# Kernel optimization log

Measured on AMD Instinct MI355X. Metric: run time of the kernel, lower is better.

The kernel has to match this reference:

```python
import jax, jax.numpy as jnp
import numpy as np

DIM = 180; HEADS = 6; WS = 16; NUM_TOKENS = 64; RDIM = 10; CAT = 128
KS = 5; MLP_HID = 360; DTD = 64; Hh = 64; Ww = 64; B = 8; M = 64


def _ln(x, g, b, eps=1e-5):
    mu = x.mean(-1, keepdims=True)
    var = ((x - mu) ** 2).mean(-1, keepdims=True)
    return (x - mu) / jnp.sqrt(var + eps) * g + b


def _l2norm(x):
    return x / jnp.clip(jnp.linalg.norm(x, axis=-1, keepdims=True), 1e-12)


def setup_inputs() -> dict:
    key = jax.random.key(0)
    ks = jax.random.split(key, 24)
    rn = lambda k, s: jax.random.normal(k, s, jnp.float32) * 0.02
    z = lambda *s: jnp.zeros(s, jnp.float32)
    return {
        'x': jax.random.normal(ks[0], (B, Hh * Ww, DIM), jnp.float32),
        'td': jax.random.normal(ks[1], (B, M, DIM), jnp.float32),
        'norm1_g': jnp.ones((DIM,), jnp.float32), 'norm1_b': z(DIM),
        'wqkv_w': rn(ks[2], (DIM, 3 * DIM)), 'wqkv_b': z(3 * DIM),
        'atd_wq_w': rn(ks[3], (DIM, RDIM)), 'atd_wq_b': z(RDIM),
        'atd_wk_w': rn(ks[4], (DIM, RDIM)), 'atd_wk_b': z(RDIM),
        'atd_wv_w': rn(ks[5], (DIM, DIM)), 'atd_wv_b': z(DIM),
        'atd_scale': jnp.ones((1,), jnp.float32),
        'aca_proj_w': rn(ks[6], (DIM, DIM)), 'aca_proj_b': z(DIM),
        'win_rpb': rn(ks[7], ((2 * WS - 1) ** 2, HEADS)),
        'win_proj_w': rn(ks[8], (DIM, DIM)), 'win_proj_b': z(DIM),
        'fc_td_w': rn(ks[9], (DIM, DTD)), 'fc_td_b': z(DTD),
        'fc1_w': rn(ks[10], (DIM, MLP_HID)), 'fc1_b': z(MLP_HID),
        'dw_w': rn(ks[11], (MLP_HID + DTD, 1, KS, KS)), 'dw_b': z(MLP_HID + DTD),
        'fc2_w': rn(ks[12], (MLP_HID + DTD, DIM)), 'fc2_b': z(DIM),
        'norm2_g': jnp.ones((DIM,), jnp.float32), 'norm2_b': z(DIM),
        'rpi_sa': jax.random.randint(ks[13], (WS * WS, WS * WS), 0, (2 * WS - 1) ** 2),
        'h': Hh, 'w': Ww,
    }


def reference(x, td, norm1_g, norm1_b, wqkv_w, wqkv_b, atd_wq_w, atd_wq_b,
              atd_wk_w, atd_wk_b, atd_wv_w, atd_wv_b, atd_scale,
              aca_proj_w, aca_proj_b, win_rpb, win_proj_w, win_proj_b,
              fc_td_w, fc_td_b, fc1_w, fc1_b, dw_w, dw_b, fc2_w, fc2_b,
              norm2_g, norm2_b, rpi_sa, h, w):
    b, n, c = x.shape
    hd = c // HEADS
    shortcut = x
    xn = _ln(x, norm1_g, norm1_b)
    qkv = xn @ wqkv_w + wqkv_b  # [b, n, 3c]

    # --- ATD_CA: l2-normalized cross-attention to token dictionary ---
    q = xn @ atd_wq_w + atd_wq_b          # [b, n, rd]
    kk = td @ atd_wk_w + atd_wk_b         # [b, m, rd]
    vv = td @ atd_wv_w + atd_wv_b         # [b, m, c]
    logit_scale = 1.0 + jnp.clip(atd_scale, 0.0, 3.0) * np.log(NUM_TOKENS)
    sim = jnp.einsum('bnr,bmr->bnm', _l2norm(q), _l2norm(kk)) * logit_scale
    attn_atd = jax.nn.softmax(sim, axis=-1)
    x_atd = jnp.einsum('bnm,bmc->bnc', attn_atd, vv)
    tk_id = jnp.argmax(attn_atd, axis=-1)  # [b, n]

    # --- AC_MSA: category-sorted grouped attention ---
    gs = min(n, CAT); ng = (n + gs - 1) // gs; pad_n = ng * gs - n
    sort_idx = jnp.argsort(tk_id, axis=-1)
    inv_idx = jnp.argsort(sort_idx, axis=-1)  # inverse permutation
    sq = jnp.take_along_axis(qkv, sort_idx[:, :, None], axis=1)
    sq = jnp.concatenate([sq, jnp.flip(sq[:, n - pad_n:n, :], axis=1)], axis=1)
    g = sq.reshape(b, ng, gs, 3, HEADS, hd).transpose(3, 0, 1, 4, 2, 5)
    qa, ka, va = g[0], g[1], g[2]          # [b, ng, H, gs, hd]
    a = jax.nn.softmax(jnp.einsum('bgHid,bgHjd->bgHij', qa, ka) * hd ** -0.5, axis=-1)
    y = jnp.einsum('bgHij,bgHjd->bgHid', a, va).transpose(0, 1, 3, 2, 4)
    y = y.reshape(b, n + pad_n, c)[:, :n]
    x_aca = jnp.take_along_axis(y, inv_idx[:, :, None], axis=1) @ aca_proj_w + aca_proj_b

    # --- gather per-token dictionary features for FFN ---
    td_proj = td @ fc_td_w + fc_td_b       # [b, m, dtd]
    x_td = jnp.take_along_axis(td_proj, jnp.broadcast_to(tk_id[:, :, None], (b, n, DTD)), axis=1)

    # --- window attention (shift_size = 0, no mask) ---
    nwh, nww = h // WS, w // WS
    win = qkv.reshape(b, nwh, WS, nww, WS, 3 * c).transpose(0, 1, 3, 2, 4, 5)
    win = win.reshape(-1, WS * WS, 3 * c)
    B_ = win.shape[0]; N = WS * WS
    wq = win.reshape(B_, N, 3, HEADS, hd).transpose(2, 0, 3, 1, 4)
    qw, kw, vw = wq[0] * hd ** -0.5, wq[1], wq[2]
    bias = win_rpb[rpi_sa.reshape(-1)].reshape(N, N, HEADS).transpose(2, 0, 1)[None]
    aw = jax.nn.softmax(jnp.einsum('wHid,wHjd->wHij', qw, kw) + bias, axis=-1)
    ow = jnp.einsum('wHij,wHjd->wHid', aw, vw).transpose(0, 2, 1, 3).reshape(B_, N, c)
    ow = ow @ win_proj_w + win_proj_b
    attn_x = ow.reshape(b, nwh, nww, WS, WS, c).transpose(0, 1, 3, 2, 4, 5).reshape(b, n, c)

    x = shortcut + x_atd + attn_x + x_aca

    # --- ConvFFN_td with depthwise conv branch ---
    x2 = _ln(x, norm2_g, norm2_b)
    h1 = jax.nn.gelu(x2 @ fc1_w + fc1_b, approximate=False)
    hc = jnp.concatenate([h1, x_td], axis=-1)  # [b, n, C]
    C = hc.shape[-1]
    img = jnp.swapaxes(hc, 1, 2).reshape(b, C, h, w)
    conv = jax.lax.conv_general_dilated(img, dw_w, (1, 1), 'SAME',
        dimension_numbers=('NCHW', 'OIHW', 'NCHW'), feature_group_count=C)
    conv = jax.nn.gelu(conv + dw_b[None, :, None, None], approximate=False)
    hc = hc + jnp.swapaxes(conv.reshape(b, C, n), 1, 2)
    return x + hc @ fc2_w + fc2_b
```

## Files before the change

### kernel.cpp

```cpp
#include <hip/hip_runtime.h>
#include <hip/hip_bf16.h>
#include <math.h>

#define BB      8
#define NTOK    4096
#define CDIM    180
#define C3      540
#define NHEADS  6
#define HD      30
#define MDICT   64
#define RD      10
#define DTD     64
#define MHID    360
#define CCAT    424
#define WS      16
#define WIN_N   256
#define GS      128
#define NG      32
#define ROWS    (BB*NTOK)
#define KP1     192
#define KP2     448

typedef __hip_bfloat16 bf16;
typedef short v8s __attribute__((ext_vector_type(8)));
typedef float f32x4 __attribute__((ext_vector_type(4)));
typedef unsigned int u32x4 __attribute__((ext_vector_type(4)));

__device__ __forceinline__ float gelu_exact(float x) {
    return 0.5f * x * (1.0f + erff(x * 0.70710678118654752f));
}
__device__ __forceinline__ float wave_sum(float v) {
    #pragma unroll
    for (int off = 32; off > 0; off >>= 1) v += __shfl_xor(v, off, 64);
    return v;
}
__device__ __forceinline__ unsigned short f2b(float v) {
    unsigned u = __float_as_uint(v);
    return (unsigned short)((u + 0x7FFFu + ((u >> 16) & 1u)) >> 16);
}
__device__ __forceinline__ float b2f(unsigned short h) {
    return __uint_as_float(((unsigned)h) << 16);
}
__device__ __forceinline__ unsigned packbf(float lo, float hi) {
    return (unsigned)f2b(lo) | ((unsigned)f2b(hi) << 16);
}

__global__ __launch_bounds__(256) void detect_kernel(const void* __restrict__ x,
                                                     int* __restrict__ flag,
                                                     int* __restrict__ diag)
{
    __shared__ int cnt;
    if (threadIdx.x == 0) { cnt = 0; *diag = 0; }
    __syncthreads();
    const unsigned short* u = (const unsigned short*)x;
    int c = 0;
    for (int i = threadIdx.x; i < 2048; i += 256) {
        unsigned short e = u[2 * i] & 0x7F80;
        if (e >= 0x4300) c++;
    }
    atomicAdd(&cnt, c);
    __syncthreads();
    if (threadIdx.x == 0) *flag = (cnt > 16) ? 1 : 0;
}

#define NCVT 23
struct CvtArgs {
    const void* src[NCVT];
    float* dst[NCVT];
    int cum[NCVT + 1];
};
__global__ __launch_bounds__(256) void convert_all_kernel(CvtArgs a, int total,
        const int* __restrict__ flag)
{
    int i = blockIdx.x * 256 + threadIdx.x;
    if (i >= total) return;
    int s = 0;
    while (i >= a.cum[s + 1]) s++;
    int off = i - a.cum[s];
    if (*flag) a.dst[s][off] = ((const float*)a.src[s])[off];
    else       a.dst[s][off] = __bfloat162float(((const bf16*)a.src[s])[off]);
}

__global__ __launch_bounds__(256) void check_f32_kernel(const float* __restrict__ buf,
        int n, int bit, int* __restrict__ diag)
{
    int i = blockIdx.x * 256 + threadIdx.x;
    if (i >= n) return;
    unsigned u = __float_as_uint(buf[i]);
    if ((u & 0x7F800000u) == 0x7F800000u) atomicOr(diag, bit);
}

__global__ __launch_bounds__(256) void emit_kernel(const float* __restrict__ src,
        void* __restrict__ out, const int* __restrict__ flag,
        const int* __restrict__ diag, int n)
{
    int i = blockIdx.x * 256 + threadIdx.x;
    if (i >= n) return;
    float v = src[i];
    int d = *diag;
    if (d) v = 100.f + 32.f * (float)d;
    if (*flag) ((float*)out)[i] = v;
    else       ((bf16*)out)[i]  = __float2bfloat16(v);
}

__global__ __launch_bounds__(256) void zero_tail_kernel(bf16* __restrict__ buf)
{
    int idx = blockIdx.x * 256 + threadIdx.x;
    int row = idx / 12, c = idx % 12;
    buf[(size_t)row * KP1 + CDIM + c] = __float2bfloat16(0.f);
}

__global__ __launch_bounds__(256) void packW_kernel(const void* __restrict__ W,
        bf16* __restrict__ Wt, int K, int N, int Kpad, int total,
        const int* __restrict__ flag)
{
    int idx = blockIdx.x * 256 + threadIdx.x;
    if (idx >= total) return;
    int n = idx / Kpad, k = idx % Kpad;
    float v = 0.f;
    if (k < K && n < N) {
        size_t src = (size_t)k * N + n;
        v = (*flag) ? ((const float*)W)[src]
                    : __bfloat162float(((const bf16*)W)[src]);
    }
    Wt[idx] = __float2bfloat16(v);
}

__global__ __launch_bounds__(256) void bias_pre_kernel(const int* __restrict__ rpi,
        const float* __restrict__ rpb, float* __restrict__ bias_t)
{
    int idx = blockIdx.x * 256 + threadIdx.x;
    int h = idx >> 16, ij = idx & 65535;
    bias_t[idx] = rpb[rpi[ij] * NHEADS + h];
}

template<bool GELU_, bool ADDRES, bool BIAS_>
__global__ __launch_bounds__(256) void mgemm_kernel(
        const bf16* __restrict__ A, int lda,
        const bf16* __restrict__ Wt, int ldw,
        const float* __restrict__ bias,
        const float* __restrict__ res, int ldr,
        float* __restrict__ outF, int ldo, int N, int K)
{
    __shared__ unsigned short As[64][32];
    __shared__ unsigned short Bs[64][32];
    int tid = threadIdx.x;
    int wave = tid >> 6, lane = tid & 63;
    int quad = lane >> 4, mr = lane & 15;
    int row0 = blockIdx.y * 64, col0 = blockIdx.x * 64;
    f32x4 z = {0.f, 0.f, 0.f, 0.f};
    f32x4 acc[4] = {z, z, z, z};
    const unsigned short* Au = (const unsigned short*)A;
    const unsigned short* Wu = (const unsigned short*)Wt;
    for (int k0 = 0; k0 < K; k0 += 32) {
        #pragma unroll
        for (int e = 0; e < 8; e++) {
            int idx = tid * 8 + e;
            int r = idx >> 5, c = idx & 31;
            As[r][c] = Au[(size_t)(row0 + r) * lda + k0 + c];
            Bs[r][c] = Wu[(size_t)(col0 + r) * ldw + k0 + c];
        }
        __syncthreads();
        v8s a;
        #pragma unroll
        for (int j = 0; j < 8; j++) a[j] = (short)As[wave * 16 + mr][quad * 8 + j];
        #pragma unroll
        for (int ni = 0; ni < 4; ni++) {
            v8s b;
            #pragma unroll
            for (int j = 0; j < 8; j++) b[j] = (short)Bs[ni * 16 + mr][quad * 8 + j];
            acc[ni] = __builtin_amdgcn_mfma_f32_16x16x32_bf16(a, b, acc[ni], 0, 0, 0);
        }
        __syncthreads();
    }
    #pragma unroll
    for (int ni = 0; ni < 4; ni++) {
        int gc = col0 + ni * 16 + mr;
        if (gc >= N) continue;
        float bv = BIAS_ ? bias[gc] : 0.f;
        #pragma unroll
        for (int r = 0; r < 4; r++) {
            int gr = row0 + wave * 16 + quad * 4 + r;
            float v = acc[ni][r] + bv;
            if (GELU_) v = gelu_exact(v);
            if (ADDRES) v += res[(size_t)gr * ldr + gc];
            outF[(size_t)gr * ldo + gc] = v;
        }
    }
}

__global__ __launch_bounds__(256) void av_mgemm_kernel(
        const bf16* __restrict__ P, const bf16* __restrict__ vvT,
        const float* __restrict__ xres, float* __restrict__ accout)
{
    __shared__ unsigned short As[64][32];
    __shared__ unsigned short Bs[64][32];
    int tid = threadIdx.x;
    int wave = tid >> 6, lane = tid & 63;
    int quad = lane >> 4, mr = lane & 15;
    int row0 = blockIdx.y * 64, col0 = blockIdx.x * 64;
    int bz = blockIdx.z;
    const unsigned short* Au = (const unsigned short*)P + (size_t)bz * NTOK * MDICT;
    const unsigned short* Wu = (const unsigned short*)vvT + (size_t)bz * 192 * MDICT;
    const float* res = xres + (size_t)bz * NTOK * CDIM;
    float* outF = accout + (size_t)bz * NTOK * CDIM;
    f32x4 z = {0.f, 0.f, 0.f, 0.f};
    f32x4 acc[4] = {z, z, z, z};
    for (int k0 = 0; k0 < MDICT; k0 += 32) {
        #pragma unroll
        for (int e = 0; e < 8; e++) {
            int idx = tid * 8 + e;
            int r = idx >> 5, c = idx & 31;
            As[r][c] = Au[(size_t)(row0 + r) * MDICT + k0 + c];
            Bs[r][c] = Wu[(size_t)(col0 + r) * MDICT + k0 + c];
        }
        __syncthreads();
        v8s a;
        #pragma unroll
        for (int j = 0; j < 8; j++) a[j] = (short)As[wave * 16 + mr][quad * 8 + j];
        #pragma unroll
        for (int ni = 0; ni < 4; ni++) {
            v8s b;
            #pragma unroll
            for (int j = 0; j < 8; j++) b[j] = (short)Bs[ni * 16 + mr][quad * 8 + j];
            acc[ni] = __builtin_amdgcn_mfma_f32_16x16x32_bf16(a, b, acc[ni], 0, 0, 0);
        }
        __syncthreads();
    }
    #pragma unroll
    for (int ni = 0; ni < 4; ni++) {
        int gc = col0 + ni * 16 + mr;
        if (gc >= CDIM) continue;
        #pragma unroll
        for (int r = 0; r < 4; r++) {
            int gr = row0 + wave * 16 + quad * 4 + r;
            float v = acc[ni][r] + res[(size_t)gr * CDIM + gc];
            outF[(size_t)gr * CDIM + gc] = v;
        }
    }
}

__global__ __launch_bounds__(256, 4) void win_mfma_kernel(const float* __restrict__ qkv,
        const float* __restrict__ bias_t, bf16* __restrict__ outb)
{
    int b = blockIdx.y;
    int widx = blockIdx.x / NHEADS;
    int hh = blockIdx.x % NHEADS;
    int wy = widx >> 2, wx = widx & 3;
    int tid = threadIdx.x;
    int wave = tid >> 6, lane = tid & 63, quad = lane >> 4, mr = lane & 15;
    __shared__ __align__(16) unsigned short Ks[64][40];
    __shared__ __align__(16) unsigned short Vt[32][80];

    size_t brow = (size_t)b * NTOK;
    const float scq = 0.18257418583505536f;

    v8s aq[4];
    #pragma unroll
    for (int tt = 0; tt < 4; tt++) {
        int m = (wave * 4 + tt) * 16 + mr;
        int nt_ = (wy * WS + (m >> 4)) * 64 + wx * WS + (m & 15);
        const float* qrow = qkv + (brow + nt_) * C3 + hh * HD;
        #pragma unroll
        for (int jj = 0; jj < 8; jj++) {
            int d = quad * 8 + jj;
            float v = (d < HD) ? qrow[d] * scq : 0.f;
            aq[tt][jj] = (short)f2b(v);
        }
    }
    f32x4 z = {0.f, 0.f, 0.f, 0.f};
    f32x4 oacc[4][2] = {{z, z}, {z, z}, {z, z}, {z, z}};
    float m_r[4], l_r[4];
    #pragma unroll
    for (int tt = 0; tt < 4; tt++) { m_r[tt] = -3.0e38f; l_r[tt] = 0.f; }
    const float* btab = bias_t + (size_t)hh * WIN_N * WIN_N;

    for (int kc = 0; kc < WIN_N; kc += 64) {
        {
            int j = tid >> 2, dg = (tid & 3) * 8;
            int tok = kc + j;
            int nt_ = (wy * WS + (tok >> 4)) * 64 + wx * WS + (tok & 15);
            const float* krow = qkv + (brow + nt_) * C3 + CDIM + hh * HD;
            const float* vrow = qkv + (brow + nt_) * C3 + 2 * CDIM + hh * HD;
            v8s kv;
            #pragma unroll
            for (int jj = 0; jj < 8; jj++) {
                int d = dg + jj;
                float kf = (d < HD) ? krow[d] : 0.f;
                float vf = (d < HD) ? vrow[d] : 0.f;
                kv[jj] = (short)f2b(kf);
                Vt[d][j] = f2b(vf);
            }
            *(v8s*)&Ks[j][dg] = kv;
        }
        __syncthreads();
        #pragma unroll
        for (int tt = 0; tt < 4; tt++) {
            f32x4 s[4];
            #pragma unroll
            for (int nt = 0; nt < 4; nt++) {
                v8s bk = *(const v8s*)&Ks[nt * 16 + mr][quad * 8];
                s[nt] = __builtin_amdgcn_mfma_f32_16x16x32_bf16(bk, aq[tt], z, 0, 0, 0);
            }
            int qg = (wave * 4 + tt) * 16 + mr;
            const float* bi = btab + (size_t)qg * WIN_N + kc;
            float mc = -3.0e38f;
            #pragma unroll
            for (int nt = 0; nt < 4; nt++) {
                f32x4 b4 = *(const f32x4*)(bi + nt * 16 + quad * 4);
                s[nt][0] += b4[0]; s[nt][1] += b4[1];
                s[nt][2] += b4[2]; s[nt][3] += b4[3];
                mc = fmaxf(mc, fmaxf(fmaxf(s[nt][0], s[nt][1]),
                                     fmaxf(s[nt][2], s[nt][3])));
            }
            mc = fmaxf(mc, __shfl_xor(mc, 16, 64));
            mc = fmaxf(mc, __shfl_xor(mc, 32, 64));
            float mn = fmaxf(m_r[tt], mc);
            float alpha = __expf(m_r[tt] - mn);
            m_r[tt] = mn;
            float ls = 0.f;
            #pragma unroll
            for (int nt = 0; nt < 4; nt++) {
                #pragma unroll
                for (int r = 0; r < 4; r++) {
                    float pp = __expf(s[nt][r] - mn);
                    ls += pp;
                    s[nt][r] = pp;
                }
            }
            ls += __shfl_xor(ls, 16, 64);
            ls += __shfl_xor(ls, 32, 64);
            l_r[tt] = l_r[tt] * alpha + ls;
            unsigned dpk[4][2];
            #pragma unroll
            for (int nt = 0; nt < 4; nt++) {
                dpk[nt][0] = packbf(s[nt][0], s[nt][1]);
                dpk[nt][1] = packbf(s[nt][2], s[nt][3]);
            }
            #pragma unroll
            for (int r = 0; r < 4; r++) {
                float av = __shfl(alpha, quad * 4 + r, 64);
                oacc[tt][0][r] *= av;
                oacc[tt][1][r] *= av;
            }
            #pragma unroll
            for (int c = 0; c < 2; c++) {
                union { u32x4 u; v8s s8; } afu;
                #pragma unroll
                for (int t = 0; t < 4; t++) {
                    int srcl = (((quad * 2 + (t >> 1)) & 3) << 4) | mr;
                    unsigned r0 = (unsigned)__shfl((int)dpk[2 * c][t & 1], srcl, 64);
                    unsigned r1 = (unsigned)__shfl((int)dpk[2 * c + 1][t & 1], srcl, 64);
                    afu.u[t] = (quad & 2) ? r1 : r0;
                }
                #pragma unroll
                for (int dt = 0; dt < 2; dt++) {
                    v8s bv = *(const v8s*)&Vt[dt * 16 + mr][c * 32 + quad * 8];
                    oacc[tt][dt] = __builtin_amdgcn_mfma_f32_16x16x32_bf16(
                        afu.s8, bv, oacc[tt][dt], 0, 0, 0);
                }
            }
        }
        __syncthreads();
    }
    #pragma unroll
    for (int tt = 0; tt < 4; tt++) {
        float il = 1.f / l_r[tt];
        #pragma unroll
        for (int r = 0; r < 4; r++) {
            float ilr = __shfl(il, quad * 4 + r, 64);
            int m = (wave * 4 + tt) * 16 + quad * 4 + r;
            int nt_ = (wy * WS + (m >> 4)) * 64 + wx * WS + (m & 15);
            #pragma unroll
            for (int dt = 0; dt < 2; dt++) {
                int d = dt * 16 + mr;
                if (d >= HD) continue;
                outb[(brow + nt_) * KP1 + hh * HD + d] =
                    __float2bfloat16(oacc[tt][dt][r] * ilr);
            }
        }
    }
}

__global__ __launch_bounds__(256) void acmsa_mfma_kernel(const float* __restrict__ qkv,
        const int* __restrict__ sidx, bf16* __restrict__ outb)
{
    int b = blockIdx.y;
    int g = blockIdx.x / NHEADS;
    int hh = blockIdx.x % NHEADS;
    int tid = threadIdx.x;
    int wave = tid >> 6, lane = tid & 63, quad = lane >> 4, mr = lane & 15;
    __shared__ int toks[GS];
    __shared__ __align__(16) unsigned short Ks[64][40];
    __shared__ __align__(16) unsigned short Vt[32][80];
    __shared__ __align__(16) unsigned short Sc[GS][72];
    __shared__ float alpha_s[GS];
    __shared__ float invl_s[GS];

    size_t brow = (size_t)b * NTOK;
    if (tid < GS) toks[tid] = sidx[brow + (size_t)g * GS + tid];
    __syncthreads();
    const float scq = 0.18257418583505536f;

    v8s aq[2];
    #pragma unroll
    for (int tt = 0; tt < 2; tt++) {
        int m = (wave * 2 + tt) * 16 + mr;
        const float* qrow = qkv + (brow + toks[m]) * C3 + hh * HD;
        #pragma unroll
        for (int jj = 0; jj < 8; jj++) {
            int d = quad * 8 + jj;
            float v = (d < HD) ? qrow[d] * scq : 0.f;
            aq[tt][jj] = (short)f2b(v);
        }
    }
    f32x4 z = {0.f, 0.f, 0.f, 0.f};
    f32x4 oacc[2][2] = {{z, z}, {z, z}};
    float m_r = -3.0e38f, l_r = 0.f;

    for (int kc = 0; kc < GS; kc += 64) {
        {
            int j = tid >> 2, dg = (tid & 3) * 8;
            int tok = toks[kc + j];
            const float* krow = qkv + (brow + tok) * C3 + CDIM + hh * HD;
            const float* vrow = qkv + (brow + tok) * C3 + 2 * CDIM + hh * HD;
            v8s kv;
            #pragma unroll
            for (int jj = 0; jj < 8; jj++) {
                int d = dg + jj;
                float kf = (d < HD) ? krow[d] : 0.f;
                float vf = (d < HD) ? vrow[d] : 0.f;
                kv[jj] = (short)f2b(kf);
                Vt[d][j] = f2b(vf);
            }
            *(v8s*)&Ks[j][dg] = kv;
        }
        __syncthreads();
        #pragma unroll
        for (int nt = 0; nt < 4; nt++) {
            v8s bk = *(const v8s*)&Ks[nt * 16 + mr][quad * 8];
            #pragma unroll
            for (int tt = 0; tt < 2; tt++) {
                f32x4 s = __builtin_amdgcn_mfma_f32_16x16x32_bf16(aq[tt], bk, z, 0, 0, 0);
                int rowb = (wave * 2 + tt) * 16 + quad * 4;
                #pragma unroll
                for (int r = 0; r < 4; r++)
                    Sc[rowb + r][nt * 16 + mr] = f2b(s[r]);
            }
        }
        __syncthreads();
        if (tid < GS) {
            int r = tid;
            float mc = -3.0e38f;
            #pragma unroll
            for (int j0 = 0; j0 < 64; j0 += 8) {
                v8s sv = *(const v8s*)&Sc[r][j0];
                #pragma unroll
                for (int jj = 0; jj < 8; jj++)
                    mc = fmaxf(mc, b2f((unsigned short)sv[jj]));
            }
            float mn = fmaxf(m_r, mc);
            float alpha = __expf(m_r - mn);
            float lsum = 0.f;
            #pragma unroll
            for (int j0 = 0; j0 < 64; j0 += 8) {
                v8s sv = *(const v8s*)&Sc[r][j0];
                v8s pv;
                #pragma unroll
                for (int jj = 0; jj < 8; jj++) {
                    float pp = __expf(b2f((unsigned short)sv[jj]) - mn);
                    lsum += pp;
                    pv[jj] = (short)f2b(pp);
                }
                *(v8s*)&Sc[r][j0] = pv;
            }
            l_r = l_r * alpha + lsum;
            m_r = mn;
            alpha_s[r] = alpha;
        }
        __syncthreads();
        #pragma unroll
        for (int tt = 0; tt < 2; tt++) {
            int rowb = (wave * 2 + tt) * 16 + quad * 4;
            float a0 = alpha_s[rowb], a1 = alpha_s[rowb + 1],
                  a2 = alpha_s[rowb + 2], a3 = alpha_s[rowb + 3];
            #pragma unroll
            for (int dt = 0; dt < 2; dt++) {
                oacc[tt][dt][0] *= a0; oacc[tt][dt][1] *= a1;
                oacc[tt][dt][2] *= a2; oacc[tt][dt][3] *= a3;
            }
        }
        #pragma unroll
        for (int kk = 0; kk < 64; kk += 32) {
            v8s ap[2];
            #pragma unroll
            for (int tt = 0; tt < 2; tt++)
                ap[tt] = *(const v8s*)&Sc[(wave * 2 + tt) * 16 + mr][kk + quad * 8];
            #pragma unroll
            for (int dt = 0; dt < 2; dt++) {
                v8s bv = *(const v8s*)&Vt[dt * 16 + mr][kk + quad * 8];
                #pragma unroll
                for (int tt = 0; tt < 2; tt++)
                    oacc[tt][dt] = __builtin_amdgcn_mfma_f32_16x16x32_bf16(
                        ap[tt], bv, oacc[tt][dt], 0, 0, 0);
            }
        }
        __syncthreads();
    }
    if (tid < GS) invl_s[tid] = 1.f / l_r;
    __syncthreads();
    #pragma unroll
    for (int tt = 0; tt < 2; tt++) {
        int rowb = (wave * 2 + tt) * 16 + quad * 4;
        #pragma unroll
        for (int dt = 0; dt < 2; dt++) {
            int d = dt * 16 + mr;
            if (d >= HD) continue;
            #pragma unroll
            for (int r = 0; r < 4; r++) {
                int m = rowb + r;
                int tok = toks[m];
                outb[(brow + tok) * KP1 + hh * HD + d] =
                    __float2bfloat16(oacc[tt][dt][r] * invl_s[m]);
            }
        }
    }
}

__global__ __launch_bounds__(64) void ln_kernel(const float* __restrict__ x,
        const float* __restrict__ g, const float* __restrict__ be,
        float* __restrict__ out, bf16* __restrict__ outb)
{
    int row = blockIdx.x; int t = threadIdx.x;
    const float* xr = x + (size_t)row * CDIM;
    float v0 = xr[t];
    float v1 = xr[t + 64];
    float v2 = (t < CDIM - 128) ? xr[t + 128] : 0.f;
    float s1 = wave_sum(v0 + v1 + v2);
    float s2 = wave_sum(v0*v0 + v1*v1 + v2*v2);
    float mu = s1 / (float)CDIM;
    float var = s2 / (float)CDIM - mu * mu;
    float rs = rsqrtf(var + 1e-5f);
    float o0 = (v0 - mu) * rs * g[t]      + be[t];
    float o1 = (v1 - mu) * rs * g[t + 64] + be[t + 64];
    float o2 = (t < CDIM - 128) ? ((v2 - mu) * rs * g[t + 128] + be[t + 128]) : 0.f;
    float* o = out + (size_t)row * CDIM;
    o[t] = o0; o[t + 64] = o1;
    if (t < CDIM - 128) o[t + 128] = o2;
    bf16* ob = outb + (size_t)row * KP1;
    ob[t]       = __float2bfloat16(o0);
    ob[t + 64]  = __float2bfloat16(o1);
    ob[t + 128] = __float2bfloat16(o2);
}

__global__ __launch_bounds__(64) void td_pre_kernel(const float* __restrict__ td,
        const float* __restrict__ wk, const float* __restrict__ wkb,
        const float* __restrict__ wv, const float* __restrict__ wvb,
        const float* __restrict__ wtd, const float* __restrict__ wtdb,
        float* __restrict__ kkn, bf16* __restrict__ vvT, float* __restrict__ tdp)
{
    int blk = blockIdx.x;
    int b = blk >> 6, m = blk & 63;
    int t = threadIdx.x;
    __shared__ float tr[CDIM];
    __shared__ float sk[RD];
    __shared__ float snorm;
    const float* tdr = td + (size_t)blk * CDIM;
    tr[t] = tdr[t]; tr[t + 64] = tdr[t + 64];
    if (t < CDIM - 128) tr[t + 128] = tdr[t + 128];
    __syncthreads();
    if (t < RD) {
        float s = wkb[t];
        for (int k = 0; k < CDIM; k++) s += tr[k] * wk[k * RD + t];
        sk[t] = s;
    }
    __syncthreads();
    if (t == 0) {
        float s = 0.f;
        #pragma unroll
        for (int j = 0; j < RD; j++) s += sk[j] * sk[j];
        snorm = fmaxf(sqrtf(s), 1e-12f);
    }
    __syncthreads();
    if (t < RD) kkn[(size_t)blk * RD + t] = sk[t] / snorm;
    for (int c = t; c < 192; c += 64) {
        float s = 0.f;
        if (c < CDIM) {
            s = wvb[c];
            for (int k = 0; k < CDIM; k++) s += tr[k] * wv[k * CDIM + c];
        }
        vvT[((size_t)(b * 192 + c)) * MDICT + m] = __float2bfloat16(s);
    }
    {
        float s = wtdb[t];
        for (int k = 0; k < CDIM; k++) s += tr[k] * wtd[k * DTD + t];
        tdp[(size_t)blk * DTD + t] = s;
    }
}

__global__ __launch_bounds__(64) void atd_soft_kernel(const float* __restrict__ xn,
        const float* __restrict__ wq, const float* __restrict__ wqb,
        const float* __restrict__ scale_p, const float* __restrict__ kkn,
        bf16* __restrict__ Pout, int* __restrict__ tk_id)
{
    int row = blockIdx.x;
    int b = row >> 12;
    int t = threadIdx.x;
    const float* xrow = xn + (size_t)row * CDIM;
    float v0 = xrow[t];
    float v1 = xrow[t + 64];
    float v2 = (t < CDIM - 128) ? xrow[t + 128] : 0.f;
    float sq[RD];
    #pragma unroll
    for (int j = 0; j < RD; j++) {
        float part = v0 * wq[t * RD + j] + v1 * wq[(t + 64) * RD + j];
        if (t < CDIM - 128) part += v2 * wq[(t + 128) * RD + j];
        sq[j] = wave_sum(part) + wqb[j];
    }
    float qn = 0.f;
    #pragma unroll
    for (int j = 0; j < RD; j++) qn += sq[j] * sq[j];
    qn = fmaxf(sqrtf(qn), 1e-12f);
    float ls = 1.0f + fminf(fmaxf(scale_p[0], 0.f), 3.f) * 4.158883083359672f;
    const float* kr = kkn + ((size_t)b * MDICT + t) * RD;
    float s = 0.f;
    #pragma unroll
    for (int j = 0; j < RD; j++) s += sq[j] * kr[j];
    s = s / qn * ls;
    float mv = s; int mi = t;
    #pragma unroll
    for (int off = 32; off > 0; off >>= 1) {
        float ov = __shfl_xor(mv, off, 64);
        int   oi = __shfl_xor(mi, off, 64);
        if (ov > mv || (ov == mv && oi < mi)) { mv = ov; mi = oi; }
    }
    float e = __expf(s - mv);
    float denom = wave_sum(e);
    Pout[(size_t)row * MDICT + t] = __float2bfloat16(e / denom);
    if (t == 0) tk_id[row] = mi;
}

__global__ __launch_bounds__(256) void sort_kernel(const int* __restrict__ tk_id,
                                                   int* __restrict__ sidx)
{
    int b = blockIdx.x; int tid = threadIdx.x;
    __shared__ int keys[NTOK];
    __shared__ int cnt[256];
    __shared__ int off[256];
    const int* kb = tk_id + (size_t)b * NTOK;
    for (int i = tid; i < NTOK; i += 256) keys[i] = kb[i];
    __syncthreads();
    int v = tid >> 2, seg = tid & 3;
    int lo = seg * 1024, hi = lo + 1024;
    int c = 0;
    for (int i = lo; i < hi; i++) c += (keys[i] == v);
    cnt[tid] = c;
    __syncthreads();
    if (tid == 0) {
        int run = 0;
        for (int l = 0; l < 256; l++) { off[l] = run; run += cnt[l]; }
    }
    __syncthreads();
    int o = off[tid];
    int* sb = sidx + (size_t)b * NTOK;
    for (int i = lo; i < hi; i++) if (keys[i] == v) sb[o++] = i;
}

__global__ __launch_bounds__(256) void gather_td_kernel(const int* __restrict__ tk_id,
        const float* __restrict__ tdp, float* __restrict__ hc)
{
    int idx = blockIdx.x * 256 + threadIdx.x;
    int row = idx >> 6, j = idx & 63;
    int b = row >> 12;
    int tk = tk_id[row];
    hc[(size_t)row * CCAT + MHID + j] = tdp[((size_t)b * MDICT + tk) * DTD + j];
}

#define CHK2 16
#define CHP2 17
__global__ __launch_bounds__(256) void conv_kernel(const float* __restrict__ hc,
        const float* __restrict__ w, const float* __restrict__ wb,
        bf16* __restrict__ outb)
{
    int ch0 = blockIdx.x * CHK2;
    int tile = blockIdx.y;
    int b = blockIdx.z;
    int ty0 = (tile >> 2) * 16, tx0 = (tile & 3) * 16;
    __shared__ float sh[400][CHP2];
    __shared__ float wt[CHK2][26];
    int tid = threadIdx.x;
    for (int idx = tid; idx < 400 * CHK2; idx += 256) {
        int pix = idx >> 4, ch = idx & (CHK2 - 1);
        int gy = ty0 + pix / 20 - 2, gx = tx0 + pix % 20 - 2;
        int chg = ch0 + ch;
        float v = 0.f;
        if (gy >= 0 && gy < 64 && gx >= 0 && gx < 64 && chg < CCAT)
            v = hc[((size_t)b * NTOK + gy * 64 + gx) * CCAT + chg];
        sh[pix][ch] = v;
    }
    for (int idx = tid; idx < CHK2 * 25; idx += 256) {
        int ch = idx / 25, kk = idx % 25;
        int chg = ch0 + ch;
        wt[ch][kk] = (chg < CCAT) ? w[chg * 25 + kk] : 0.f;
    }
    __syncthreads();
    int px = tid & 15, py = tid >> 4;
    size_t obase = ((size_t)b * NTOK + (ty0 + py) * 64 + tx0 + px) * KP2;
    #pragma unroll
    for (int ch = 0; ch < CHK2; ch++) {
        int chg = ch0 + ch;
        float v = 0.f;
        if (chg < CCAT) {
            float a = 0.f;
            #pragma unroll
            for (int dy = 0; dy < 5; dy++)
                #pragma unroll
                for (int dx = 0; dx < 5; dx++)
                    a += sh[(py + dy) * 20 + px + dx][ch] * wt[ch][dy * 5 + dx];
            float gv = gelu_exact(a + wb[chg]);
            v = sh[(py + 2) * 20 + px + 2][ch] + gv;
        }
        outb[obase + chg] = __float2bfloat16(v);
    }
}

extern "C" void kernel_launch(void* const* d_in, const int* in_sizes, int n_in,
                              void* d_out, int out_size, void* d_ws, size_t ws_size,
                              hipStream_t stream)
{
    (void)n_in; (void)ws_size; (void)out_size;
    const int* rpi = (const int*)d_in[28];

    float* p = (float*)d_ws;
    float* xn    = p; p += (size_t)ROWS * CDIM;
    float* acc   = p; p += (size_t)ROWS * CDIM;
    float* tmp1  = p; p += (size_t)ROWS * CDIM;
    float* qkv   = p; p += (size_t)ROWS * C3;
    float* hcnew = p; p += (size_t)ROWS * CCAT;
    float* kkn   = p; p += (size_t)BB * MDICT * RD;
    bf16*  vvT   = (bf16*)p; p += (size_t)BB * 192 * MDICT / 2;
    float* tdp   = p; p += (size_t)BB * MDICT * DTD;
    int*   tk_id = (int*)p; p += ROWS;
    int*   sidx  = (int*)p; p += ROWS;
    int*   flag  = (int*)p; p += 64;
    int*   diag  = (int*)p; p += 64;
    bf16* wtqkv = (bf16*)p; p += 576 * KP1 / 2;
    bf16* wtaca = (bf16*)p; p += 192 * KP1 / 2;
    bf16* wtwin = (bf16*)p; p += 192 * KP1 / 2;
    bf16* wtfc1 = (bf16*)p; p += 384 * KP1 / 2;
    bf16* wtfc2 = (bf16*)p; p += 192 * KP2 / 2;
    float* cin[28];
    for (int i = 0; i < 28; i++) { cin[i] = p; p += in_sizes[i]; }
    float* bias_t = p; p += (size_t)NHEADS * WIN_N * WIN_N;

    float* hc      = qkv;
    bf16*  xnb     = (bf16*)hcnew;
    bf16*  tmp1b   = (bf16*)(hcnew + (size_t)ROWS * KP1 / 2);
    bf16*  hcnewb2 = (bf16*)hcnew;
    bf16*  Pbuf    = (bf16*)tmp1;

    detect_kernel<<<1, 256, 0, stream>>>(d_in[0], flag, diag);
    {
        CvtArgs ca;
        int total = 0, s = 0;
        for (int i = 0; i < 28; i++) {
            if (i == 4 || i == 13 || i == 16 || i == 20 || i == 24) continue;
            ca.src[s] = d_in[i];
            ca.dst[s] = cin[i];
            ca.cum[s] = total;
            total += in_sizes[i];
            s++;
        }
        ca.cum[s] = total;
        convert_all_kernel<<<(total + 255) / 256, 256, 0, stream>>>(ca, total, flag);
    }
    const float *x = cin[0], *td = cin[1], *n1g = cin[2], *n1b = cin[3],
        *wqkv_b = cin[5], *wq_w = cin[6], *wq_b = cin[7],
        *wk_w = cin[8], *wk_b = cin[9], *wv_w = cin[10], *wv_b = cin[11],
        *atd_scale = cin[12], *aca_b = cin[14], *win_rpb = cin[15],
        *winp_b = cin[17], *fctd_w = cin[18], *fctd_b = cin[19],
        *fc1_b = cin[21], *dw_w = cin[22], *dw_b = cin[23], *fc2_b = cin[25],
        *n2g = cin[26], *n2b = cin[27];

    packW_kernel<<<576 * KP1 / 256, 256, 0, stream>>>(d_in[4],  wtqkv, CDIM, C3,   KP1, 576 * KP1, flag);
    packW_kernel<<<192 * KP1 / 256, 256, 0, stream>>>(d_in[13], wtaca, CDIM, CDIM, KP1, 192 * KP1, flag);
    packW_kernel<<<192 * KP1 / 256, 256, 0, stream>>>(d_in[16], wtwin, CDIM, CDIM, KP1, 192 * KP1, flag);
    packW_kernel<<<384 * KP1 / 256, 256, 0, stream>>>(d_in[20], wtfc1, CDIM, MHID, KP1, 384 * KP1, flag);
    packW_kernel<<<192 * KP2 / 256, 256, 0, stream>>>(d_in[24], wtfc2, CCAT, CDIM, KP2, 192 * KP2, flag);
    bias_pre_kernel<<<NHEADS * WIN_N * WIN_N / 256, 256, 0, stream>>>(rpi, win_rpb, bias_t);

    td_pre_kernel<<<BB * MDICT, 64, 0, stream>>>(td, wk_w, wk_b, wv_w, wv_b,
                                                 fctd_w, fctd_b, kkn, vvT, tdp);
    ln_kernel<<<ROWS, 64, 0, stream>>>(x, n1g, n1b, xn, xnb);
    mgemm_kernel<false, false, true><<<dim3(9, ROWS / 64), 256, 0, stream>>>(
        xnb, KP1, wtqkv, KP1, wqkv_b, nullptr, 0, qkv, C3, C3, KP1);
    atd_soft_kernel<<<ROWS, 64, 0, stream>>>(xn, wq_w, wq_b, atd_scale, kkn, Pbuf, tk_id);
    av_mgemm_kernel<<<dim3(3, NTOK / 64, BB), 256, 0, stream>>>(Pbuf, vvT, x, acc);
    sort_kernel<<<BB, 256, 0, stream>>>(tk_id, sidx);
    zero_tail_kernel<<<ROWS * 12 / 256, 256, 0, stream>>>(tmp1b);
    acmsa_mfma_kernel<<<dim3(NG * NHEADS, BB), 256, 0, stream>>>(qkv, sidx, tmp1b);
    mgemm_kernel<false, true, true><<<dim3(3, ROWS / 64), 256, 0, stream>>>(
        tmp1b, KP1, wtaca, KP1, aca_b, acc, CDIM, acc, CDIM, CDIM, KP1);
    win_mfma_kernel<<<dim3(16 * NHEADS, BB), 256, 0, stream>>>(qkv, bias_t, tmp1b);
    mgemm_kernel<false, true, true><<<dim3(3, ROWS / 64), 256, 0, stream>>>(
        tmp1b, KP1, wtwin, KP1, winp_b, acc, CDIM, acc, CDIM, CDIM, KP1);
    ln_kernel<<<ROWS, 64, 0, stream>>>(acc, n2g, n2b, xn, xnb);
    mgemm_kernel<true, false, true><<<dim3(6, ROWS / 64), 256, 0, stream>>>(
        xnb, KP1, wtfc1, KP1, fc1_b, nullptr, 0, hc, CCAT, MHID, KP1);
    gather_td_kernel<<<ROWS * 64 / 256, 256, 0, stream>>>(tk_id, tdp, hc);
    conv_kernel<<<dim3(28, 16, BB), 256, 0, stream>>>(hc, dw_w, dw_b, hcnewb2);
    mgemm_kernel<false, true, true><<<dim3(3, ROWS / 64), 256, 0, stream>>>(
        hcnewb2, KP2, wtfc2, KP2, fc2_b, acc, CDIM, tmp1, CDIM, CDIM, KP2);
    check_f32_kernel<<<(ROWS * CDIM + 255) / 256, 256, 0, stream>>>(tmp1, ROWS * CDIM, 8, diag);
    emit_kernel<<<(ROWS * CDIM + 255) / 256, 256, 0, stream>>>(
        tmp1, d_out, flag, diag, ROWS * CDIM);
}
```

Measured before the change: 726.9 us.

## Retile depthwise conv to 8x8 pixels by 64 channels with vectorized bf16 stores

Each conv block now covers an 8x8 spatial tile and 64 channels instead of a 16x16 tile and 16 channels. Each thread keeps 16 channel accumulators for one pixel and writes them as two packed 8-element bf16 vector stores. The goal is wider, channel-contiguous global loads and fewer, larger output stores. The cost is a larger halo ratio: each block loads 144 pixels to produce 64, where before it loaded 400 to produce 256. It also uses more registers per thread.

```diff
diff --git a/kernel.cpp b/kernel.cpp
--- a/kernel.cpp
+++ b/kernel.cpp
@@ -676,52 +676,71 @@
     hc[(size_t)row * CCAT + MHID + j] = tdp[((size_t)b * MDICT + tk) * DTD + j];
 }
 
-#define CHK2 16
-#define CHP2 17
+#define CHK3 64
+#define CTW  8
+#define CTH  8
+#define CHW  12
+#define CHP  144
+#define CSP  65
 __global__ __launch_bounds__(256) void conv_kernel(const float* __restrict__ hc,
         const float* __restrict__ w, const float* __restrict__ wb,
         bf16* __restrict__ outb)
 {
-    int ch0 = blockIdx.x * CHK2;
+    int ch0 = blockIdx.x * CHK3;
     int tile = blockIdx.y;
     int b = blockIdx.z;
-    int ty0 = (tile >> 2) * 16, tx0 = (tile & 3) * 16;
-    __shared__ float sh[400][CHP2];
-    __shared__ float wt[CHK2][26];
+    int ty0 = (tile >> 3) * CTH, tx0 = (tile & 7) * CTW;
+    __shared__ float sh[CHP][CSP];
+    __shared__ float wt[25][CHK3];
     int tid = threadIdx.x;
-    for (int idx = tid; idx < 400 * CHK2; idx += 256) {
-        int pix = idx >> 4, ch = idx & (CHK2 - 1);
-        int gy = ty0 + pix / 20 - 2, gx = tx0 + pix % 20 - 2;
+    for (int idx = tid; idx < CHP * CHK3; idx += 256) {
+        int pix = idx >> 6, ch = idx & 63;
+        int gy = ty0 + pix / CHW - 2, gx = tx0 + pix % CHW - 2;
         int chg = ch0 + ch;
         float v = 0.f;
         if (gy >= 0 && gy < 64 && gx >= 0 && gx < 64 && chg < CCAT)
             v = hc[((size_t)b * NTOK + gy * 64 + gx) * CCAT + chg];
         sh[pix][ch] = v;
     }
-    for (int idx = tid; idx < CHK2 * 25; idx += 256) {
-        int ch = idx / 25, kk = idx % 25;
+    for (int idx = tid; idx < 25 * CHK3; idx += 256) {
+        int kk = idx >> 6, ch = idx & 63;
         int chg = ch0 + ch;
-        wt[ch][kk] = (chg < CCAT) ? w[chg * 25 + kk] : 0.f;
-    }
-    __syncthreads();
-    int px = tid & 15, py = tid >> 4;
-    size_t obase = ((size_t)b * NTOK + (ty0 + py) * 64 + tx0 + px) * KP2;
-    #pragma unroll
-    for (int ch = 0; ch < CHK2; ch++) {
-        int chg = ch0 + ch;
+        wt[kk][ch] = (chg < CCAT) ? w[chg * 25 + kk] : 0.f;
+    }
+    __syncthreads();
+    int q = tid & 3, p = tid >> 2;
+    int px = p & 7, py = p >> 3;
+    int cb = q * 16;
+    float acc[16];
+    #pragma unroll
+    for (int c = 0; c < 16; c++) acc[c] = 0.f;
+    #pragma unroll
+    for (int dy = 0; dy < 5; dy++) {
+        #pragma unroll
+        for (int dx = 0; dx < 5; dx++) {
+            const float* sp = &sh[(py + dy) * CHW + px + dx][cb];
+            const float* wp = &wt[dy * 5 + dx][cb];
+            #pragma unroll
+            for (int c = 0; c < 16; c++) acc[c] += sp[c] * wp[c];
+        }
+    }
+    const float* cp = &sh[(py + 2) * CHW + px + 2][cb];
+    v8s pk0, pk1;
+    #pragma unroll
+    for (int c = 0; c < 16; c++) {
+        int chg = ch0 + cb + c;
         float v = 0.f;
         if (chg < CCAT) {
-            float a = 0.f;
-            #pragma unroll
-            for (int dy = 0; dy < 5; dy++)
-                #pragma unroll
-                for (int dx = 0; dx < 5; dx++)
-                    a += sh[(py + dy) * 20 + px + dx][ch] * wt[ch][dy * 5 + dx];
-            float gv = gelu_exact(a + wb[chg]);
-            v = sh[(py + 2) * 20 + px + 2][ch] + gv;
-        }
-        outb[obase + chg] = __float2bfloat16(v);
-    }
+            float gv = gelu_exact(acc[c] + wb[chg]);
+            v = cp[c] + gv;
+        }
+        if (c < 8) pk0[c] = (short)f2b(v);
+        else       pk1[c - 8] = (short)f2b(v);
+    }
+    size_t obase = ((size_t)b * NTOK + (ty0 + py) * 64 + tx0 + px) * KP2 + ch0 + cb;
+    unsigned short* ob = (unsigned short*)outb + obase;
+    *(v8s*)ob = pk0;
+    *(v8s*)(ob + 8) = pk1;
 }
 
 extern "C" void kernel_launch(void* const* d_in, const int* in_sizes, int n_in,
@@ -808,7 +827,7 @@
     mgemm_kernel<true, false, true><<<dim3(6, ROWS / 64), 256, 0, stream>>>(
         xnb, KP1, wtfc1, KP1, fc1_b, nullptr, 0, hc, CCAT, MHID, KP1);
     gather_td_kernel<<<ROWS * 64 / 256, 256, 0, stream>>>(tk_id, tdp, hc);
-    conv_kernel<<<dim3(28, 16, BB), 256, 0, stream>>>(hc, dw_w, dw_b, hcnewb2);
+    conv_kernel<<<dim3(7, 64, BB), 256, 0, stream>>>(hc, dw_w, dw_b, hcnewb2);
     mgemm_kernel<false, true, true><<<dim3(3, ROWS / 64), 256, 0, stream>>>(
         hcnewb2, KP2, wtfc2, KP2, fc2_b, acc, CDIM, tmp1, CDIM, CDIM, KP2);
     check_f32_kernel<<<(ROWS * CDIM + 255) / 256, 256, 0, stream>>>(tmp1, ROWS * CDIM, 8, diag);
```

Result: slower. 1.426 ms (+96.2%).
